# Optimization experiments

Measured on AMD Instinct MI355X. Metric: run time of the kernel, lower is better.

Reference implementation:

```python
import jax, jax.numpy as jnp
import numpy as np

N_NODES = 4_000_000
N_GRAPHS = 4096  # B; fixed for jit (torch derives it from batch.max()+1)
D_FEAT = 8
NUM_CLASSES = 10


def setup_inputs() -> dict:
    key = jax.random.key(0)
    k1, k2, k3, k4, k5 = jax.random.split(key, 5)
    x = jax.random.normal(k1, (N_NODES, D_FEAT), dtype=jnp.float32)
    # sorted segment ids; with ~977 nodes/graph expected, empty segments are vanishingly unlikely
    batch_ids = jnp.sort(jax.random.randint(k2, (N_NODES,), 0, N_GRAPHS, dtype=jnp.int64))
    input_ids = jax.random.randint(k3, (N_GRAPHS, 128), 0, 30522, dtype=jnp.int64)
    attention_mask = jnp.ones((N_GRAPHS, 128), dtype=jnp.int64)
    W = jax.random.normal(k4, (NUM_CLASSES, D_FEAT), dtype=jnp.float32) * (1.0 / np.sqrt(D_FEAT))
    b = jax.random.normal(k5, (NUM_CLASSES,), dtype=jnp.float32) * 0.01
    return {"x": x, "batch_ids": batch_ids, "input_ids": input_ids,
            "attention_mask": attention_mask, "W": W, "b": b}


def reference(x, batch_ids, input_ids, attention_mask, W, b):
    # Segment-mean pooling: replaces the O(B) python loop of masked means
    # with a single-pass scatter-add. input_ids / attention_mask are unused
    # by the original forward (kept for signature fidelity).
    sums = jax.ops.segment_sum(x, batch_ids, num_segments=N_GRAPHS)          # [B, 8]
    counts = jax.ops.segment_sum(jnp.ones((x.shape[0],), x.dtype), batch_ids,
                                 num_segments=N_GRAPHS)                      # [B]
    pooled = sums / counts[:, None]                                          # [B, 8]
    logits = pooled @ W.T + b                                                # [B, 10]
    return logits
```

## Files before the change

### kernel.cpp

```cpp
#include <hip/hip_runtime.h>

constexpr int N_NODES  = 4000000;
constexpr int N_GRAPHS = 4096;
constexpr int D_FEAT   = 8;
constexpr int N_CLS    = 10;
constexpr int GPB      = 4;
constexpr int WIN      = 8192;

typedef float f32x4 __attribute__((ext_vector_type(4)));

__global__ __launch_bounds__(256) void fused_all(
    const float* __restrict__ x,
    const int*   __restrict__ ids,
    const float* __restrict__ W,
    const float* __restrict__ bias,
    float*       __restrict__ out)
{
    const f32x4* xf = (const f32x4*)x;
    int g0   = blockIdx.x * GPB;
    int wid  = threadIdx.x >> 6;
    int lane = threadIdx.x & 63;
    int half = lane >> 5;
    int l32  = lane & 31;
    int target = g0 + half * GPB;

    int est = (int)((long long)target * N_NODES / N_GRAPHS);
    int lo = est - WIN; if (lo < 0) lo = 0;
    int hi = est + WIN; if (hi > N_NODES) hi = N_NODES;
    {
        bool okL = (lo == 0)       || (ids[lo - 1] < target);
        bool okR = (hi == N_NODES) || (ids[hi] >= target);
        if (!(okL && okR)) { lo = 0; hi = N_NODES; }
    }

    while (hi - lo > 32) {
        int chunk = (hi - lo + 31) >> 5;
        int pos = lo + l32 * chunk;
        int v = (pos < hi) ? ids[pos] : 0x7fffffff;
        unsigned long long m = __ballot(v < target);
        unsigned int mm = half ? (unsigned int)(m >> 32) : (unsigned int)m;
        int cnt = __popc(mm);
        int nlo = cnt ? lo + (cnt - 1) * chunk + 1 : lo;
        int nhi = (cnt < 32) ? min(lo + cnt * chunk, hi) : hi;
        lo = nlo; hi = nhi;
    }
    {
        int pos = lo + l32;
        int v = (pos < hi) ? ids[pos] : 0x7fffffff;
        unsigned long long m = __ballot(v < target);
        unsigned int mm = half ? (unsigned int)(m >> 32) : (unsigned int)m;
        lo += __popc(mm);
    }
    int s = __shfl(lo, 0);
    int e = __shfl(lo, 32);

    __shared__ int lb[GPB + 1];
    if (threadIdx.x < GPB + 1) lb[threadIdx.x] = -1;
    __syncthreads();
    if (threadIdx.x == 0) { lb[0] = s; lb[GPB] = e; }
    for (int i = s + 1 + (int)threadIdx.x; i < e; i += 256) {
        int cur  = ids[i];
        int prev = ids[i - 1];
        if (cur != prev) {
            for (int k = prev + 1; k <= cur; ++k) lb[k - g0] = i;
        }
    }
    __syncthreads();
    if (threadIdx.x == 0) {
        for (int k = GPB - 1; k >= 1; --k) if (lb[k] < 0) lb[k] = lb[k + 1];
    }
    __syncthreads();

    int gs = lb[wid];
    int ge = lb[wid + 1];

    f32x4 a0 = (f32x4)(0.f), a1 = (f32x4)(0.f),
          a2 = (f32x4)(0.f), a3 = (f32x4)(0.f);
    int i    = 2 * gs + lane;
    int endf = 2 * ge;
    int full = (endf - 2 * gs) >> 8;
    for (int it = 0; it < full; ++it, i += 256) {
        a0 += xf[i];
        a1 += xf[i +  64];
        a2 += xf[i + 128];
        a3 += xf[i + 192];
    }
    for (; i < endf; i += 64) a0 += xf[i];
    f32x4 acc = (a0 + a1) + (a2 + a3);

    #pragma unroll
    for (int off = 32; off >= 2; off >>= 1) {
        acc.x += __shfl_xor(acc.x, off);
        acc.y += __shfl_xor(acc.y, off);
        acc.z += __shfl_xor(acc.z, off);
        acc.w += __shfl_xor(acc.w, off);
    }
    float m0 = __shfl(acc.x, 0), m1 = __shfl(acc.y, 0);
    float m2 = __shfl(acc.z, 0), m3 = __shfl(acc.w, 0);
    float m4 = __shfl(acc.x, 1), m5 = __shfl(acc.y, 1);
    float m6 = __shfl(acc.z, 1), m7 = __shfl(acc.w, 1);

    if (lane < N_CLS) {
        float inv = 1.0f / (float)(ge - gs);
        const float* w = W + (size_t)lane * D_FEAT;
        float a = bias[lane];
        a += (m0 * inv) * w[0] + (m1 * inv) * w[1]
           + (m2 * inv) * w[2] + (m3 * inv) * w[3]
           + (m4 * inv) * w[4] + (m5 * inv) * w[5]
           + (m6 * inv) * w[6] + (m7 * inv) * w[7];
        out[(size_t)(g0 + wid) * N_CLS + lane] = a;
    }
}

extern "C" void kernel_launch(void* const* d_in, const int* in_sizes, int n_in,
                              void* d_out, int out_size, void* d_ws, size_t ws_size,
                              hipStream_t stream) {
    const float* x   = (const float*)d_in[0];
    const int*   ids = (const int*)d_in[1];
    const float* W   = (const float*)d_in[4];
    const float* b   = (const float*)d_in[5];
    float*       out = (float*)d_out;

    fused_all<<<N_GRAPHS / GPB, 256, 0, stream>>>(x, ids, W, b, out);
}
```

Measured before the change: 32.52 us.

## Replace per-block binary search with grid-wide boundary scan and cooperative grid sync

Rather than having each block binary-search the sorted segment ids, every thread scans the whole id array with vectorized loads and writes segment start offsets to a workspace buffer. A grid-wide cooperative sync follows, after which each wavefront reads its graph's bounds and reduces its rows as before. This removes the search latency chain but adds a full 16MB read of ids, global scattered writes, and a grid barrier, and it needs a cooperative launch of 1024 blocks to be co-resident.

```diff
diff --git a/kernel.cpp b/kernel.cpp
--- a/kernel.cpp
+++ b/kernel.cpp
@@ -1,84 +1,59 @@
 #include <hip/hip_runtime.h>
+#include <hip/hip_cooperative_groups.h>
+
+namespace cg = cooperative_groups;
 
 constexpr int N_NODES  = 4000000;
 constexpr int N_GRAPHS = 4096;
 constexpr int D_FEAT   = 8;
 constexpr int N_CLS    = 10;
-constexpr int GPB      = 4;
-constexpr int WIN      = 8192;
+constexpr int NBLK     = 1024;
+constexpr int NTHREADS = 256;
 
 typedef float f32x4 __attribute__((ext_vector_type(4)));
+typedef int   i32x4 __attribute__((ext_vector_type(4)));
 
-__global__ __launch_bounds__(256) void fused_all(
+__global__ __launch_bounds__(256) void fused_coop(
     const float* __restrict__ x,
     const int*   __restrict__ ids,
     const float* __restrict__ W,
     const float* __restrict__ bias,
-    float*       __restrict__ out)
+    float*       __restrict__ out,
+    int*         __restrict__ bounds)
 {
-    const f32x4* xf = (const f32x4*)x;
-    int g0   = blockIdx.x * GPB;
+    const f32x4* xf   = (const f32x4*)x;
+    const i32x4* ids4 = (const i32x4*)ids;
+    int tid  = blockIdx.x * blockDim.x + threadIdx.x;
+    int nthr = NBLK * NTHREADS;
+
+    for (int t = tid; t < N_NODES / 4; t += nthr) {
+        int base = t * 4;
+        i32x4 v = ids4[t];
+        int prev = (base == 0) ? -1 : ids[base - 1];
+        int cur;
+        cur = v.x; if (cur != prev) { for (int g = prev + 1; g <= cur; ++g) bounds[g] = base + 0; } prev = cur;
+        cur = v.y; if (cur != prev) { for (int g = prev + 1; g <= cur; ++g) bounds[g] = base + 1; } prev = cur;
+        cur = v.z; if (cur != prev) { for (int g = prev + 1; g <= cur; ++g) bounds[g] = base + 2; } prev = cur;
+        cur = v.w; if (cur != prev) { for (int g = prev + 1; g <= cur; ++g) bounds[g] = base + 3; } prev = cur;
+        if (base + 4 >= N_NODES) {
+            for (int g = prev + 1; g <= N_GRAPHS; ++g) bounds[g] = N_NODES;
+        }
+    }
+
+    cg::this_grid().sync();
+
     int wid  = threadIdx.x >> 6;
     int lane = threadIdx.x & 63;
-    int half = lane >> 5;
-    int l32  = lane & 31;
-    int target = g0 + half * GPB;
+    int g    = blockIdx.x * 4 + wid;
 
-    int est = (int)((long long)target * N_NODES / N_GRAPHS);
-    int lo = est - WIN; if (lo < 0) lo = 0;
-    int hi = est + WIN; if (hi > N_NODES) hi = N_NODES;
-    {
-        bool okL = (lo == 0)       || (ids[lo - 1] < target);
-        bool okR = (hi == N_NODES) || (ids[hi] >= target);
-        if (!(okL && okR)) { lo = 0; hi = N_NODES; }
-    }
-
-    while (hi - lo > 32) {
-        int chunk = (hi - lo + 31) >> 5;
-        int pos = lo + l32 * chunk;
-        int v = (pos < hi) ? ids[pos] : 0x7fffffff;
-        unsigned long long m = __ballot(v < target);
-        unsigned int mm = half ? (unsigned int)(m >> 32) : (unsigned int)m;
-        int cnt = __popc(mm);
-        int nlo = cnt ? lo + (cnt - 1) * chunk + 1 : lo;
-        int nhi = (cnt < 32) ? min(lo + cnt * chunk, hi) : hi;
-        lo = nlo; hi = nhi;
-    }
-    {
-        int pos = lo + l32;
-        int v = (pos < hi) ? ids[pos] : 0x7fffffff;
-        unsigned long long m = __ballot(v < target);
-        unsigned int mm = half ? (unsigned int)(m >> 32) : (unsigned int)m;
-        lo += __popc(mm);
-    }
-    int s = __shfl(lo, 0);
-    int e = __shfl(lo, 32);
-
-    __shared__ int lb[GPB + 1];
-    if (threadIdx.x < GPB + 1) lb[threadIdx.x] = -1;
-    __syncthreads();
-    if (threadIdx.x == 0) { lb[0] = s; lb[GPB] = e; }
-    for (int i = s + 1 + (int)threadIdx.x; i < e; i += 256) {
-        int cur  = ids[i];
-        int prev = ids[i - 1];
-        if (cur != prev) {
-            for (int k = prev + 1; k <= cur; ++k) lb[k - g0] = i;
-        }
-    }
-    __syncthreads();
-    if (threadIdx.x == 0) {
-        for (int k = GPB - 1; k >= 1; --k) if (lb[k] < 0) lb[k] = lb[k + 1];
-    }
-    __syncthreads();
-
-    int gs = lb[wid];
-    int ge = lb[wid + 1];
+    int s = bounds[g];
+    int e = bounds[g + 1];
 
     f32x4 a0 = (f32x4)(0.f), a1 = (f32x4)(0.f),
           a2 = (f32x4)(0.f), a3 = (f32x4)(0.f);
-    int i    = 2 * gs + lane;
-    int endf = 2 * ge;
-    int full = (endf - 2 * gs) >> 8;
+    int i    = 2 * s + lane;
+    int endf = 2 * e;
+    int full = (endf - 2 * s) >> 8;
     for (int it = 0; it < full; ++it, i += 256) {
         a0 += xf[i];
         a1 += xf[i +  64];
@@ -101,14 +76,14 @@
     float m6 = __shfl(acc.z, 1), m7 = __shfl(acc.w, 1);
 
     if (lane < N_CLS) {
-        float inv = 1.0f / (float)(ge - gs);
+        float inv = 1.0f / (float)(e - s);
         const float* w = W + (size_t)lane * D_FEAT;
         float a = bias[lane];
         a += (m0 * inv) * w[0] + (m1 * inv) * w[1]
            + (m2 * inv) * w[2] + (m3 * inv) * w[3]
            + (m4 * inv) * w[4] + (m5 * inv) * w[5]
            + (m6 * inv) * w[6] + (m7 * inv) * w[7];
-        out[(size_t)(g0 + wid) * N_CLS + lane] = a;
+        out[(size_t)g * N_CLS + lane] = a;
     }
 }
 
@@ -120,6 +95,11 @@
     const float* W   = (const float*)d_in[4];
     const float* b   = (const float*)d_in[5];
     float*       out = (float*)d_out;
+    int*         bounds = (int*)d_ws;
 
-    fused_all<<<N_GRAPHS / GPB, 256, 0, stream>>>(x, ids, W, b, out);
+    void* args[] = { (void*)&x, (void*)&ids, (void*)&W, (void*)&b,
+                     (void*)&out, (void*)&bounds };
+    hipLaunchCooperativeKernel((const void*)fused_coop,
+                               dim3(NBLK), dim3(NTHREADS),
+                               args, 0, stream);
 }
```

Measured after the change: 88.30 us. +171.5%, slower.
